# Kernel tuning notes

Hardware: AMD Instinct MI355X
Metric: run time of the kernel (lower is better)

The kernel has to match this reference:

```python
import jax, jax.numpy as jnp
import numpy as np

N_NODES = 50000
N_EDGES = 800000
F_IN = 128
HEADS = 4
HEAD_DIM = 32  # hidden_size // heads
HIDDEN = HEADS * HEAD_DIM
N_GRAPHS = 64
LEAKY_SLOPE = 0.01
EPS_LN = 1e-5


def setup_inputs() -> dict:
    key = jax.random.key(0)
    ks = jax.random.split(key, 12)
    x = jax.random.normal(ks[0], (N_NODES, F_IN), dtype=jnp.float32)
    edge_index = jax.random.randint(ks[1], (2, N_EDGES), 0, N_NODES, dtype=jnp.int64)
    batch = jnp.sort(jax.random.randint(ks[2], (N_NODES,), 0, N_GRAPHS, dtype=jnp.int64))
    s = 1.0 / np.sqrt(F_IN).astype(np.float32)
    Wq = jax.random.normal(ks[3], (F_IN, HIDDEN), dtype=jnp.float32) * s
    bq = jnp.zeros((HIDDEN,), jnp.float32)
    Wk = jax.random.normal(ks[4], (F_IN, HIDDEN), dtype=jnp.float32) * s
    bk = jnp.zeros((HIDDEN,), jnp.float32)
    Wv = jax.random.normal(ks[5], (F_IN, HIDDEN), dtype=jnp.float32) * s
    bv = jnp.zeros((HIDDEN,), jnp.float32)
    Ws = jax.random.normal(ks[6], (F_IN, HIDDEN), dtype=jnp.float32) * s  # root/skip lin
    bs = jnp.zeros((HIDDEN,), jnp.float32)
    ln_w = jnp.ones((HIDDEN,), jnp.float32)
    ln_b = jnp.zeros((HIDDEN,), jnp.float32)
    return {"x": x, "edge_index": edge_index, "batch": batch,
            "Wq": Wq, "bq": bq, "Wk": Wk, "bk": bk, "Wv": Wv, "bv": bv,
            "Ws": Ws, "bs": bs, "ln_w": ln_w, "ln_b": ln_b}


def reference(x, edge_index, batch, Wq, bq, Wk, bk, Wv, bv, Ws, bs, ln_w, ln_b):
    N = x.shape[0]
    src, dst = edge_index[0], edge_index[1]  # message j(src) -> i(dst)
    q = (x @ Wq + bq).reshape(N, HEADS, HEAD_DIM)
    k = (x @ Wk + bk).reshape(N, HEADS, HEAD_DIM)
    v = (x @ Wv + bv).reshape(N, HEADS, HEAD_DIM)
    # per-edge attention logits [E, H]
    alpha = jnp.einsum('ehc,ehc->eh', q[dst], k[src]) / jnp.sqrt(jnp.float32(HEAD_DIM))
    # scatter-softmax over incoming edges of each destination node
    m = jax.ops.segment_max(alpha, dst, num_segments=N)
    m = jnp.where(jnp.isfinite(m), m, 0.0)  # empty segments -> -inf; neutralize
    ex = jnp.exp(alpha - m[dst])
    denom = jax.ops.segment_sum(ex, dst, num_segments=N)
    attn = ex / (denom[dst] + 1e-16)
    # scatter-add aggregation of weighted values, concat heads
    out = jax.ops.segment_sum(attn[:, :, None] * v[src], dst, num_segments=N)
    out = out.reshape(N, HIDDEN) + x @ Ws + bs  # root/skip connection
    # PyG graph-mode LayerNorm: normalize over all nodes+channels of each graph
    cnt = jax.ops.segment_sum(jnp.ones((N,), out.dtype), batch, num_segments=N_GRAPHS)
    norm = jnp.maximum(cnt, 1.0) * HIDDEN
    mean = jax.ops.segment_sum(out.sum(-1), batch, num_segments=N_GRAPHS) / norm
    outc = out - mean[batch][:, None]
    var = jax.ops.segment_sum((outc * outc).sum(-1), batch, num_segments=N_GRAPHS) / norm
    y = outc / jnp.sqrt(var + EPS_LN)[batch][:, None]
    y = y * ln_w + ln_b
    y = jnp.where(y > 0, y, LEAKY_SLOPE * y)  # LeakyReLU
    return (y, attn)
```

## Files before the change

kernel.cpp:

```cpp
#include <hip/hip_runtime.h>
#include <hip/hip_fp16.h>

constexpr int N_NODES = 50000;
constexpr int N_EDGES = 800000;
constexpr int HIDDEN  = 128;
constexpr float RSQRT_D = 0.17677669529663687f;
constexpr int Y_SIZE = N_NODES * HIDDEN;
constexpr int M_PAD  = 50048;
constexpr int SCAN_BLOCKS = 196;
constexpr int XCVT_BLOCKS = (M_PAD * 16) / 256;
constexpr int HIST_BLOCKS = N_EDGES / 256;

constexpr size_t OFF_Q      = 0;
constexpr size_t OFF_K      = 6400000;
constexpr size_t OFF_V      = 12800000;
constexpr size_t OFF_S      = 19200000;
constexpr size_t OFF_DENOM  = 25600000;
constexpr size_t OFF_GSUM   = 25800000;
constexpr size_t OFF_GSQ    = 25800064;
constexpr size_t OFF_GCNT   = 25800128;
constexpr size_t OFF_DEG    = 25800192;
constexpr size_t OFF_OFFS   = 25850192;
constexpr size_t OFF_CURSOR = 25900224;
constexpr size_t OFF_CSR    = 25950224;
constexpr size_t OFF_PART   = 27550224;

typedef __attribute__((ext_vector_type(8))) short bf16x8;
typedef __attribute__((ext_vector_type(4))) float f32x4;

__device__ __forceinline__ short f2bf(float f) {
    unsigned u = __float_as_uint(f);
    unsigned r = (u + 0x7fff + ((u >> 16) & 1)) >> 16;
    return (short)r;
}

__device__ __forceinline__ void gload_lds16(const void* g, void* l) {
    __builtin_amdgcn_global_load_lds(
        (const __attribute__((address_space(1))) void*)g,
        (__attribute__((address_space(3))) void*)l, 16, 0, 0);
}

__global__ __launch_bounds__(256) void k_prep(
    const float* __restrict__ x,
    const float* __restrict__ Wq, const float* __restrict__ Wk,
    const float* __restrict__ Wv, const float* __restrict__ Wsm,
    const int* __restrict__ dst,
    short* __restrict__ xs, short* __restrict__ wt, int* __restrict__ deg)
{
    int b = blockIdx.x;
    if (b < XCVT_BLOCKS) {
        int tid = b * 256 + threadIdx.x;
        int row = tid >> 4, ci = tid & 15;
        short o[8];
        if (row < N_NODES) {
            float4 a = *(const float4*)&x[(size_t)row * 128 + ci * 8];
            float4 bb = *(const float4*)&x[(size_t)row * 128 + ci * 8 + 4];
            o[0] = f2bf(a.x); o[1] = f2bf(a.y); o[2] = f2bf(a.z); o[3] = f2bf(a.w);
            o[4] = f2bf(bb.x); o[5] = f2bf(bb.y); o[6] = f2bf(bb.z); o[7] = f2bf(bb.w);
        } else {
            #pragma unroll
            for (int j = 0; j < 8; ++j) o[j] = 0;
        }
        int cs = ci ^ (row & 7);
        *(int4*)&xs[(size_t)row * 128 + cs * 8] = *(int4*)o;
    } else if (b < XCVT_BLOCKS + 32) {
        int tid = (b - XCVT_BLOCKS) * 256 + threadIdx.x;
        int mat = tid >> 11, n = (tid >> 4) & 127, kg = tid & 15;
        const float* W = (mat == 0) ? Wq : (mat == 1) ? Wk : (mat == 2) ? Wv : Wsm;
        short o[8];
        #pragma unroll
        for (int j = 0; j < 8; ++j) o[j] = f2bf(W[(kg * 8 + j) * 128 + n]);
        int cs = kg ^ (n & 7);
        *(int4*)&wt[mat * 16384 + n * 128 + cs * 8] = *(int4*)o;
    } else {
        int e = (b - XCVT_BLOCKS - 32) * 256 + threadIdx.x;
        atomicAdd(&deg[dst[e]], 1);
    }
}

__global__ __launch_bounds__(256) void k_mm(
    const short* __restrict__ xs, const short* __restrict__ wt,
    const float* __restrict__ bq, const float* __restrict__ bk,
    const float* __restrict__ bv, const float* __restrict__ bs,
    __half* __restrict__ qb, __half* __restrict__ kv, __half* __restrict__ sb)
{
    __shared__ __align__(16) char As[32768];
    __shared__ __align__(16) char Bs[32768];
    const int t = threadIdx.x, lane = t & 63, wv = t >> 6;
    const int m0 = blockIdx.x * 128;
    const int wm = wv >> 1, wn = wv & 1;

    const char* gA = (const char*)xs + (size_t)m0 * 256;
    #pragma unroll
    for (int i = 0; i < 8; ++i) {
        int chunk = wv * 8 + i;
        gload_lds16(gA + chunk * 1024 + lane * 16, As + chunk * 1024);
        gload_lds16((const char*)wt + chunk * 1024 + lane * 16, Bs + chunk * 1024);
    }
    __syncthreads();

    bf16x8 af[4][4];
    #pragma unroll
    for (int ks = 0; ks < 4; ++ks) {
        const int cbase = ks * 64 + ((lane >> 4) << 4);
        #pragma unroll
        for (int mf = 0; mf < 4; ++mf) {
            int mr = wm * 64 + mf * 16 + (lane & 15);
            af[ks][mf] = *(const bf16x8*)(As + mr * 256 + (cbase ^ ((mr & 7) << 4)));
        }
    }

    const float* Bbs[4] = {bq, bk, bv, bs};
    #pragma unroll
    for (int mat = 0; mat < 4; ++mat) {
        f32x4 acc[4][4];
        #pragma unroll
        for (int nf = 0; nf < 4; ++nf) {
            float bc = Bbs[mat][wn * 64 + nf * 16 + (lane & 15)];
            #pragma unroll
            for (int mf = 0; mf < 4; ++mf) acc[mf][nf] = (f32x4){bc, bc, bc, bc};
        }
        #pragma unroll
        for (int ks = 0; ks < 4; ++ks) {
            bf16x8 bfr[4];
            const int cbase = ks * 64 + ((lane >> 4) << 4);
            #pragma unroll
            for (int nf = 0; nf < 4; ++nf) {
                int nc = wn * 64 + nf * 16 + (lane & 15);
                bfr[nf] = *(const bf16x8*)(Bs + nc * 256 + (cbase ^ ((nc & 7) << 4)));
            }
            #pragma unroll
            for (int mf = 0; mf < 4; ++mf)
                #pragma unroll
                for (int nf = 0; nf < 4; ++nf)
                    acc[mf][nf] = __builtin_amdgcn_mfma_f32_16x16x32_bf16(
                        af[ks][mf], bfr[nf], acc[mf][nf], 0, 0, 0);
        }
        __syncthreads();
        if (mat < 3) {
            const char* gB = (const char*)wt + (mat + 1) * 32768;
            #pragma unroll
            for (int i = 0; i < 8; ++i) {
                int chunk = wv * 8 + i;
                gload_lds16(gB + chunk * 1024 + lane * 16, Bs + chunk * 1024);
            }
        }
        __half* base = (mat == 0) ? qb : (mat == 1) ? kv : (mat == 2) ? (kv + 128) : sb;
        const int rs = (mat == 1 || mat == 2) ? 256 : 128;
        const int colbase = wn * 64 + (lane & 15);
        #pragma unroll
        for (int mf = 0; mf < 4; ++mf) {
            int rowb = m0 + wm * 64 + mf * 16 + ((lane >> 4) << 2);
            #pragma unroll
            for (int nf = 0; nf < 4; ++nf) {
                int col = colbase + nf * 16;
                #pragma unroll
                for (int r = 0; r < 4; ++r) {
                    int node = rowb + r;
                    if (node < N_NODES)
                        base[(size_t)node * rs + col] = __float2half_rn(acc[mf][nf][r]);
                }
            }
        }
        __syncthreads();
    }
}

__global__ __launch_bounds__(256) void k_scan1(const int* __restrict__ deg,
                                               int* __restrict__ part)
{
    const int t = threadIdx.x;
    int idx = blockIdx.x * 256 + t;
    int v = (idx < N_NODES) ? deg[idx] : 0;
    #pragma unroll
    for (int o = 1; o < 64; o <<= 1) v += __shfl_xor(v, o);
    __shared__ int wsum[4];
    if ((t & 63) == 0) wsum[t >> 6] = v;
    __syncthreads();
    if (t == 0) part[blockIdx.x] = wsum[0] + wsum[1] + wsum[2] + wsum[3];
}

__global__ __launch_bounds__(256) void k_scan2(int* __restrict__ part)
{
    __shared__ int buf[256];
    const int t = threadIdx.x;
    int v = (t < SCAN_BLOCKS) ? part[t] : 0;
    buf[t] = v;
    __syncthreads();
    for (int o = 1; o < 256; o <<= 1) {
        int tmp = (t >= o) ? buf[t - o] : 0;
        __syncthreads();
        buf[t] += tmp;
        __syncthreads();
    }
    if (t < SCAN_BLOCKS) part[t] = buf[t] - v;
}

__global__ __launch_bounds__(256) void k_scan3(const int* __restrict__ deg,
                                               const int* __restrict__ part,
                                               int* __restrict__ offs,
                                               int* __restrict__ cursor)
{
    const int t = threadIdx.x;
    const int idx = blockIdx.x * 256 + t;
    const int lane = t & 63, w = t >> 6;
    int v = (idx < N_NODES) ? deg[idx] : 0;
    int inc = v;
    #pragma unroll
    for (int o = 1; o < 64; o <<= 1) {
        int nb = __shfl_up(inc, o);
        if (lane >= o) inc += nb;
    }
    __shared__ int wsum[4];
    if (lane == 63) wsum[w] = inc;
    __syncthreads();
    int wbase = 0;
    #pragma unroll
    for (int i = 0; i < 4; ++i) if (i < w) wbase += wsum[i];
    int excl = part[blockIdx.x] + wbase + inc - v;
    if (idx < N_NODES) {
        offs[idx] = excl;
        cursor[idx] = excl;
    }
    if (idx == 0) offs[N_NODES] = N_EDGES;
}

__global__ __launch_bounds__(256) void k_scatter(
    const int* __restrict__ src, const int* __restrict__ dst,
    int* __restrict__ cursor, int2* __restrict__ csr)
{
    int e = blockIdx.x * 256 + threadIdx.x;
    int d = dst[e];
    int pos = atomicAdd(&cursor[d], 1);
    csr[pos] = make_int2(src[e], e);
}

__global__ __launch_bounds__(256) void k_fused(
    const __half2* __restrict__ qb, const __half2* __restrict__ kvp,
    const __half2* __restrict__ sb,
    const int* __restrict__ offs, const int2* __restrict__ csr,
    float* __restrict__ exbuf, float* __restrict__ denom,
    float* __restrict__ outb)
{
    const int t = threadIdx.x;
    const int lane = t & 63;
    const int n = blockIdx.x * 4 + (t >> 6);
    const int begin = offs[n], end = offs[n + 1];
    const float2 qv = __half22float2(qb[(size_t)n * 64 + lane]);
    const float2 sv = __half22float2(sb[(size_t)n * 64 + lane]);
    const int h = lane >> 4;
    float acc0 = 0.f, acc1 = 0.f, dsum = 0.f;
    int i = begin;
    for (; i + 4 <= end; i += 4) {
        int2 c[4];
        #pragma unroll
        for (int u = 0; u < 4; ++u) c[u] = csr[i + u];
        __half2 kh[4], vh[4];
        #pragma unroll
        for (int u = 0; u < 4; ++u) kh[u] = kvp[(size_t)c[u].x * 128 + lane];
        #pragma unroll
        for (int u = 0; u < 4; ++u) vh[u] = kvp[(size_t)c[u].x * 128 + 64 + lane];
        float p[4];
        #pragma unroll
        for (int u = 0; u < 4; ++u) {
            float2 kf = __half22float2(kh[u]);
            p[u] = qv.x * kf.x + qv.y * kf.y;
        }
        #pragma unroll
        for (int u = 0; u < 4; ++u) p[u] += __shfl_xor(p[u], 1);
        #pragma unroll
        for (int u = 0; u < 4; ++u) p[u] += __shfl_xor(p[u], 2);
        #pragma unroll
        for (int u = 0; u < 4; ++u) p[u] += __shfl_xor(p[u], 4);
        #pragma unroll
        for (int u = 0; u < 4; ++u) p[u] += __shfl_xor(p[u], 8);
        #pragma unroll
        for (int u = 0; u < 4; ++u) {
            float ex = __expf(p[u] * RSQRT_D);
            dsum += ex;
            float2 vf = __half22float2(vh[u]);
            acc0 += ex * vf.x;
            acc1 += ex * vf.y;
            if ((lane & 15) == 0) exbuf[c[u].y * 4 + h] = ex;
        }
    }
    for (; i < end; ++i) {
        const int2 c0 = csr[i];
        const __half2 kh0 = kvp[(size_t)c0.x * 128 + lane];
        const __half2 vh0 = kvp[(size_t)c0.x * 128 + 64 + lane];
        const float2 k0 = __half22float2(kh0);
        float p0 = qv.x * k0.x + qv.y * k0.y;
        p0 += __shfl_xor(p0, 1);
        p0 += __shfl_xor(p0, 2);
        p0 += __shfl_xor(p0, 4);
        p0 += __shfl_xor(p0, 8);
        const float ex0 = __expf(p0 * RSQRT_D);
        dsum += ex0;
        const float2 v0 = __half22float2(vh0);
        acc0 += ex0 * v0.x;
        acc1 += ex0 * v0.y;
        if ((lane & 15) == 0) exbuf[c0.y * 4 + h] = ex0;
    }
    if ((lane & 15) == 0) denom[n * 4 + h] = dsum;
    const float rdn = 1.f / (dsum + 1e-16f);
    float2 o = make_float2(acc0 * rdn + sv.x, acc1 * rdn + sv.y);
    *(float2*)&outb[(size_t)n * 128 + lane * 2] = o;
}

__global__ __launch_bounds__(256) void k_norm(
    float* __restrict__ attn, const float* __restrict__ denom,
    const int* __restrict__ dst)
{
    int idx = blockIdx.x * 256 + threadIdx.x;
    int e = idx >> 2, h = idx & 3;
    attn[idx] = attn[idx] / (denom[dst[e] * 4 + h] + 1e-16f);
}

__global__ __launch_bounds__(256) void k_stats(
    const float* __restrict__ out, const int* __restrict__ batch,
    float* __restrict__ gsum, float* __restrict__ gsq, int* __restrict__ gcnt)
{
    __shared__ float nsum[32], nsq[32];
    __shared__ int   ngr[32];
    const int t = threadIdx.x;
    const int nl = t >> 3, part = t & 7;
    const int n = blockIdx.x * 32 + nl;
    float lsum = 0.f, lsq = 0.f;
    if (n < N_NODES) {
        size_t base = (size_t)n * 128 + part * 16;
        #pragma unroll
        for (int i = 0; i < 4; ++i) {
            float4 o = *(const float4*)&out[base + i * 4];
            lsum += o.x + o.y + o.z + o.w;
            lsq  += o.x * o.x + o.y * o.y + o.z * o.z + o.w * o.w;
        }
    }
    #pragma unroll
    for (int o = 1; o < 8; o <<= 1) {
        lsum += __shfl_xor(lsum, o);
        lsq  += __shfl_xor(lsq, o);
    }
    if (part == 0) { nsum[nl] = lsum; nsq[nl] = lsq; ngr[nl] = (n < N_NODES) ? batch[n] : -1; }
    __syncthreads();
    if (t == 0) {
        float acc = 0.f, accq = 0.f; int cg = ngr[0], cnt = 0;
        for (int i = 0; i < 32; ++i) {
            int g = ngr[i];
            if (g != cg) {
                if (cg >= 0) { atomicAdd(&gsum[cg], acc); atomicAdd(&gsq[cg], accq);
                               atomicAdd(&gcnt[cg], cnt); }
                acc = 0.f; accq = 0.f; cnt = 0; cg = g;
            }
            acc += nsum[i]; accq += nsq[i]; ++cnt;
        }
        if (cg >= 0) { atomicAdd(&gsum[cg], acc); atomicAdd(&gsq[cg], accq);
                       atomicAdd(&gcnt[cg], cnt); }
    }
}

__global__ __launch_bounds__(256) void k_final(
    const float* __restrict__ out, const int* __restrict__ batch,
    const float* __restrict__ gsum, const float* __restrict__ gsq,
    const int* __restrict__ gcnt,
    const float* __restrict__ lnw, const float* __restrict__ lnb,
    float* __restrict__ y)
{
    int idx = blockIdx.x * 256 + threadIdx.x;
    int n = idx >> 7, c = idx & 127;
    int g = batch[n];
    float norm = fmaxf((float)gcnt[g], 1.f) * 128.f;
    float mean = gsum[g] / norm;
    float var  = gsq[g] / norm - mean * mean;
    float inv  = rsqrtf(var + 1e-5f);
    float val  = (out[idx] - mean) * inv * lnw[c] + lnb[c];
    y[idx] = val > 0.f ? val : 0.01f * val;
}

extern "C" void kernel_launch(void* const* d_in, const int* in_sizes, int n_in,
                              void* d_out, int out_size, void* d_ws, size_t ws_size,
                              hipStream_t stream)
{
    (void)in_sizes; (void)n_in; (void)out_size; (void)ws_size;
    const float* x    = (const float*)d_in[0];
    const int*   ei   = (const int*)  d_in[1];
    const int*   batch= (const int*)  d_in[2];
    const float* Wq   = (const float*)d_in[3];
    const float* bq   = (const float*)d_in[4];
    const float* Wk   = (const float*)d_in[5];
    const float* bk   = (const float*)d_in[6];
    const float* Wv   = (const float*)d_in[7];
    const float* bv   = (const float*)d_in[8];
    const float* Wsm  = (const float*)d_in[9];
    const float* bs   = (const float*)d_in[10];
    const float* lnw  = (const float*)d_in[11];
    const float* lnb  = (const float*)d_in[12];

    float* outp = (float*)d_out;
    float* ws   = (float*)d_ws;

    const int* srcI = ei;
    const int* dstI = ei + N_EDGES;

    __half* qb      = (__half*)(ws + OFF_Q);
    __half* kv      = (__half*)(ws + OFF_K);
    __half* sb      = (__half*)(ws + OFF_S);
    float*  denom   = ws + OFF_DENOM;
    short*  wt      = (short*)(ws + OFF_DENOM);
    float*  gsum    = ws + OFF_GSUM;
    float*  gsq     = ws + OFF_GSQ;
    int*    gcnt    = (int*)(ws + OFF_GCNT);
    int*    deg     = (int*)(ws + OFF_DEG);
    int*    offs    = (int*)(ws + OFF_OFFS);
    int*    cursor  = (int*)(ws + OFF_CURSOR);
    int2*   csr     = (int2*)(ws + OFF_CSR);
    int*    partArr = (int*)(ws + OFF_PART);

    float* outb  = outp;
    short* x_swz = (short*)outp;
    float* attn  = outp + Y_SIZE;

    hipMemsetAsync(gsum, 0, (size_t)(192 + N_NODES) * sizeof(float), stream);

    k_prep<<<XCVT_BLOCKS + 32 + HIST_BLOCKS, 256, 0, stream>>>(
        x, Wq, Wk, Wv, Wsm, dstI, x_swz, wt, deg);
    k_mm<<<M_PAD / 128, 256, 0, stream>>>(x_swz, wt, bq, bk, bv, bs, qb, kv, sb);

    k_scan1<<<SCAN_BLOCKS, 256, 0, stream>>>(deg, partArr);
    k_scan2<<<1, 256, 0, stream>>>(partArr);
    k_scan3<<<SCAN_BLOCKS, 256, 0, stream>>>(deg, partArr, offs, cursor);
    k_scatter<<<N_EDGES / 256, 256, 0, stream>>>(srcI, dstI, cursor, csr);
    k_fused<<<N_NODES / 4, 256, 0, stream>>>((const __half2*)qb, (const __half2*)kv,
                                             (const __half2*)sb, offs, csr,
                                             attn, denom, outb);
    k_norm<<<(N_EDGES * 4) / 256, 256, 0, stream>>>(attn, denom, dstI);
    k_stats<<<(N_NODES + 31) / 32, 256, 0, stream>>>(outb, batch, gsum, gsq, gcnt);
    k_final<<<Y_SIZE / 256, 256, 0, stream>>>(outb, batch, gsum, gsq, gcnt,
                                              lnw, lnb, outp);
}
```

Baseline: 240.3 us.

## Process four edges per wavefront in attention aggregation and merge norm/stats kernels

The fused attention kernel now splits each 64-lane wavefront into four 16-lane quarters, each handling a different incoming edge with 8 channels per lane. Per-edge dot products need fewer shuffles, and partial sums are combined across quarters at the end. This raises memory-level parallelism for the gathers, but a tail loop with masked lanes is needed for degrees not divisible by four. The separate attention-normalisation and LayerNorm-statistics kernels are also merged into one launch selected by block index, removing one kernel launch.

```diff
diff --git a/kernel.cpp b/kernel.cpp
--- a/kernel.cpp
+++ b/kernel.cpp
@@ -10,10 +10,11 @@
 constexpr int SCAN_BLOCKS = 196;
 constexpr int XCVT_BLOCKS = (M_PAD * 16) / 256;
 constexpr int HIST_BLOCKS = N_EDGES / 256;
+constexpr int NORM_BLOCKS = (N_EDGES * 4) / 256;
+constexpr int STAT_BLOCKS = (N_NODES + 31) / 32;
 
 constexpr size_t OFF_Q      = 0;
 constexpr size_t OFF_K      = 6400000;
-constexpr size_t OFF_V      = 12800000;
 constexpr size_t OFF_S      = 19200000;
 constexpr size_t OFF_DENOM  = 25600000;
 constexpr size_t OFF_GSUM   = 25800000;
@@ -236,8 +237,8 @@
 }
 
 __global__ __launch_bounds__(256) void k_fused(
-    const __half2* __restrict__ qb, const __half2* __restrict__ kvp,
-    const __half2* __restrict__ sb,
+    const __half* __restrict__ qb, const __half* __restrict__ kv,
+    const __half* __restrict__ sb,
     const int* __restrict__ offs, const int2* __restrict__ csr,
     float* __restrict__ exbuf, float* __restrict__ denom,
     float* __restrict__ outb)
@@ -246,85 +247,118 @@
     const int lane = t & 63;
     const int n = blockIdx.x * 4 + (t >> 6);
     const int begin = offs[n], end = offs[n + 1];
-    const float2 qv = __half22float2(qb[(size_t)n * 64 + lane]);
-    const float2 sv = __half22float2(sb[(size_t)n * 64 + lane]);
-    const int h = lane >> 4;
-    float acc0 = 0.f, acc1 = 0.f, dsum = 0.f;
+    const int cl  = lane & 15;
+    const int qtr = lane >> 4;
+    const int h   = cl >> 2;
+
+    const __half2* qp = (const __half2*)(qb + (size_t)n * 128 + cl * 8);
+    float2 qf[4];
+    #pragma unroll
+    for (int j = 0; j < 4; ++j) qf[j] = __half22float2(qp[j]);
+
+    float acc[8] = {0.f, 0.f, 0.f, 0.f, 0.f, 0.f, 0.f, 0.f};
+    float dsum = 0.f;
     int i = begin;
-    for (; i + 4 <= end; i += 4) {
-        int2 c[4];
-        #pragma unroll
-        for (int u = 0; u < 4; ++u) c[u] = csr[i + u];
-        __half2 kh[4], vh[4];
-        #pragma unroll
-        for (int u = 0; u < 4; ++u) kh[u] = kvp[(size_t)c[u].x * 128 + lane];
-        #pragma unroll
-        for (int u = 0; u < 4; ++u) vh[u] = kvp[(size_t)c[u].x * 128 + 64 + lane];
-        float p[4];
-        #pragma unroll
-        for (int u = 0; u < 4; ++u) {
-            float2 kf = __half22float2(kh[u]);
-            p[u] = qv.x * kf.x + qv.y * kf.y;
-        }
-        #pragma unroll
-        for (int u = 0; u < 4; ++u) p[u] += __shfl_xor(p[u], 1);
-        #pragma unroll
-        for (int u = 0; u < 4; ++u) p[u] += __shfl_xor(p[u], 2);
-        #pragma unroll
-        for (int u = 0; u < 4; ++u) p[u] += __shfl_xor(p[u], 4);
-        #pragma unroll
-        for (int u = 0; u < 4; ++u) p[u] += __shfl_xor(p[u], 8);
-        #pragma unroll
-        for (int u = 0; u < 4; ++u) {
-            float ex = __expf(p[u] * RSQRT_D);
-            dsum += ex;
-            float2 vf = __half22float2(vh[u]);
-            acc0 += ex * vf.x;
-            acc1 += ex * vf.y;
-            if ((lane & 15) == 0) exbuf[c[u].y * 4 + h] = ex;
-        }
-    }
-    for (; i < end; ++i) {
-        const int2 c0 = csr[i];
-        const __half2 kh0 = kvp[(size_t)c0.x * 128 + lane];
-        const __half2 vh0 = kvp[(size_t)c0.x * 128 + 64 + lane];
-        const float2 k0 = __half22float2(kh0);
-        float p0 = qv.x * k0.x + qv.y * k0.y;
+    for (; i + 8 <= end; i += 8) {
+        const int2 c0 = csr[i + qtr];
+        const int2 c1 = csr[i + 4 + qtr];
+        const __half2* k0 = (const __half2*)(kv + (size_t)c0.x * 256 + cl * 8);
+        const __half2* k1 = (const __half2*)(kv + (size_t)c1.x * 256 + cl * 8);
+        __half2 ka[4], kb2[4], va[4], vb2[4];
+        #pragma unroll
+        for (int j = 0; j < 4; ++j) { ka[j] = k0[j]; va[j] = k0[64 + j]; }
+        #pragma unroll
+        for (int j = 0; j < 4; ++j) { kb2[j] = k1[j]; vb2[j] = k1[64 + j]; }
+        float p0 = 0.f, p1 = 0.f;
+        #pragma unroll
+        for (int j = 0; j < 4; ++j) {
+            float2 f0 = __half22float2(ka[j]), f1 = __half22float2(kb2[j]);
+            p0 += qf[j].x * f0.x + qf[j].y * f0.y;
+            p1 += qf[j].x * f1.x + qf[j].y * f1.y;
+        }
+        p0 += __shfl_xor(p0, 1);  p1 += __shfl_xor(p1, 1);
+        p0 += __shfl_xor(p0, 2);  p1 += __shfl_xor(p1, 2);
+        const float ex0 = __expf(p0 * RSQRT_D);
+        const float ex1 = __expf(p1 * RSQRT_D);
+        dsum += ex0 + ex1;
+        #pragma unroll
+        for (int j = 0; j < 4; ++j) {
+            float2 f0 = __half22float2(va[j]), f1 = __half22float2(vb2[j]);
+            acc[2*j]   += ex0 * f0.x + ex1 * f1.x;
+            acc[2*j+1] += ex0 * f0.y + ex1 * f1.y;
+        }
+        if ((lane & 3) == 0) {
+            exbuf[c0.y * 4 + h] = ex0;
+            exbuf[c1.y * 4 + h] = ex1;
+        }
+    }
+    for (; i < end; i += 4) {
+        const int eIdx = i + qtr;
+        const bool act = eIdx < end;
+        const int2 c0 = csr[act ? eIdx : end - 1];
+        const __half2* k0 = (const __half2*)(kv + (size_t)c0.x * 256 + cl * 8);
+        __half2 ka[4], va[4];
+        #pragma unroll
+        for (int j = 0; j < 4; ++j) { ka[j] = k0[j]; va[j] = k0[64 + j]; }
+        float p0 = 0.f;
+        #pragma unroll
+        for (int j = 0; j < 4; ++j) {
+            float2 f0 = __half22float2(ka[j]);
+            p0 += qf[j].x * f0.x + qf[j].y * f0.y;
+        }
         p0 += __shfl_xor(p0, 1);
         p0 += __shfl_xor(p0, 2);
-        p0 += __shfl_xor(p0, 4);
-        p0 += __shfl_xor(p0, 8);
-        const float ex0 = __expf(p0 * RSQRT_D);
+        const float ex0 = act ? __expf(p0 * RSQRT_D) : 0.f;
         dsum += ex0;
-        const float2 v0 = __half22float2(vh0);
-        acc0 += ex0 * v0.x;
-        acc1 += ex0 * v0.y;
-        if ((lane & 15) == 0) exbuf[c0.y * 4 + h] = ex0;
-    }
-    if ((lane & 15) == 0) denom[n * 4 + h] = dsum;
-    const float rdn = 1.f / (dsum + 1e-16f);
-    float2 o = make_float2(acc0 * rdn + sv.x, acc1 * rdn + sv.y);
-    *(float2*)&outb[(size_t)n * 128 + lane * 2] = o;
-}
-
-__global__ __launch_bounds__(256) void k_norm(
+        #pragma unroll
+        for (int j = 0; j < 4; ++j) {
+            float2 f0 = __half22float2(va[j]);
+            acc[2*j]   += ex0 * f0.x;
+            acc[2*j+1] += ex0 * f0.y;
+        }
+        if (((lane & 3) == 0) && act) exbuf[c0.y * 4 + h] = ex0;
+    }
+    dsum += __shfl_xor(dsum, 16);
+    dsum += __shfl_xor(dsum, 32);
+    #pragma unroll
+    for (int j = 0; j < 8; ++j) {
+        acc[j] += __shfl_xor(acc[j], 16);
+        acc[j] += __shfl_xor(acc[j], 32);
+    }
+    if (lane < 16) {
+        if ((lane & 3) == 0) denom[n * 4 + h] = dsum;
+        const float rdn = 1.f / (dsum + 1e-16f);
+        const __half2* sp = (const __half2*)(sb + (size_t)n * 128 + cl * 8);
+        float o[8];
+        #pragma unroll
+        for (int j = 0; j < 4; ++j) {
+            float2 sf = __half22float2(sp[j]);
+            o[2*j]   = acc[2*j]   * rdn + sf.x;
+            o[2*j+1] = acc[2*j+1] * rdn + sf.y;
+        }
+        *(float4*)&outb[(size_t)n * 128 + cl * 8]     = make_float4(o[0], o[1], o[2], o[3]);
+        *(float4*)&outb[(size_t)n * 128 + cl * 8 + 4] = make_float4(o[4], o[5], o[6], o[7]);
+    }
+}
+
+__global__ __launch_bounds__(256) void k_post(
     float* __restrict__ attn, const float* __restrict__ denom,
-    const int* __restrict__ dst)
-{
-    int idx = blockIdx.x * 256 + threadIdx.x;
-    int e = idx >> 2, h = idx & 3;
-    attn[idx] = attn[idx] / (denom[dst[e] * 4 + h] + 1e-16f);
-}
-
-__global__ __launch_bounds__(256) void k_stats(
+    const int* __restrict__ dst,
     const float* __restrict__ out, const int* __restrict__ batch,
     float* __restrict__ gsum, float* __restrict__ gsq, int* __restrict__ gcnt)
 {
+    const int b = blockIdx.x;
+    if (b < NORM_BLOCKS) {
+        int idx = b * 256 + threadIdx.x;
+        int e = idx >> 2, h = idx & 3;
+        attn[idx] = attn[idx] / (denom[dst[e] * 4 + h] + 1e-16f);
+        return;
+    }
     __shared__ float nsum[32], nsq[32];
     __shared__ int   ngr[32];
     const int t = threadIdx.x;
     const int nl = t >> 3, part = t & 7;
-    const int n = blockIdx.x * 32 + nl;
+    const int n = (b - NORM_BLOCKS) * 32 + nl;
     float lsum = 0.f, lsq = 0.f;
     if (n < N_NODES) {
         size_t base = (size_t)n * 128 + part * 16;
@@ -429,11 +463,10 @@
     k_scan2<<<1, 256, 0, stream>>>(partArr);
     k_scan3<<<SCAN_BLOCKS, 256, 0, stream>>>(deg, partArr, offs, cursor);
     k_scatter<<<N_EDGES / 256, 256, 0, stream>>>(srcI, dstI, cursor, csr);
-    k_fused<<<N_NODES / 4, 256, 0, stream>>>((const __half2*)qb, (const __half2*)kv,
-                                             (const __half2*)sb, offs, csr,
+    k_fused<<<N_NODES / 4, 256, 0, stream>>>(qb, kv, sb, offs, csr,
                                              attn, denom, outb);
-    k_norm<<<(N_EDGES * 4) / 256, 256, 0, stream>>>(attn, denom, dstI);
-    k_stats<<<(N_NODES + 31) / 32, 256, 0, stream>>>(outb, batch, gsum, gsq, gcnt);
+    k_post<<<NORM_BLOCKS + STAT_BLOCKS, 256, 0, stream>>>(
+        attn, denom, dstI, outb, batch, gsum, gsq, gcnt);
     k_final<<<Y_SIZE / 256, 256, 0, stream>>>(outb, batch, gsum, gsq, gcnt,
                                               lnw, lnb, outp);
 }
```

Result: faster. 230.8 us (-4.0%).
